# Kernel tuning notes

Hardware: AMD Instinct MI355X
Metric: run time of the kernel (lower is better)

## Reference

```python
import jax, jax.numpy as jnp
import numpy as np

B, N, HID, HEADS, NCT, GDIM = 8, 1024, 1024, 16, 32, 128
HD = HID // HEADS  # head_dim = 64
SCALE = float(np.sqrt(HD))


def setup_inputs() -> dict:
    key = jax.random.key(0)
    ks = jax.random.split(key, 20)
    def lin(k, fan_in, shape):
        bound = 1.0 / np.sqrt(fan_in)
        return jax.random.uniform(k, shape, jnp.float32, -bound, bound)
    return {
        "x": jax.random.normal(ks[0], (B, N, HID), jnp.float32),
        "cancer_type": jax.random.randint(ks[1], (B,), 0, NCT),
        "graph_context": jax.random.normal(ks[2], (B, GDIM), jnp.float32),
        "attn_mask": jnp.zeros((B, N), dtype=bool),
        # projections (stored as [in, out] so y = x @ W + b)
        "Wq": lin(ks[3], HID, (HID, HID)), "bq": lin(ks[4], HID, (HID,)),
        "Wk": lin(ks[5], HID, (HID, HID)), "bk": lin(ks[6], HID, (HID,)),
        "Wv": lin(ks[7], HID, (HID, HID)), "bv": lin(ks[8], HID, (HID,)),
        "Wo": lin(ks[9], HID, (HID, HID)), "bo": lin(ks[10], HID, (HID,)),
        # embeddings
        "ct_bias_emb": jax.random.normal(ks[11], (NCT, HEADS), jnp.float32),
        "ct_key_emb": jax.random.normal(ks[12], (NCT, HID), jnp.float32),
        # graph_attn_bias MLP: graph_dim -> 2*heads -> heads (ELU between)
        "Wg1": lin(ks[13], GDIM, (GDIM, 2 * HEADS)), "bg1": lin(ks[14], GDIM, (2 * HEADS,)),
        "Wg2": lin(ks[15], 2 * HEADS, (2 * HEADS, HEADS)), "bg2": lin(ks[16], 2 * HEADS, (HEADS,)),
        # graph_key_mod: Linear(graph_dim, hidden) + ELU
        "Wgk": lin(ks[17], GDIM, (GDIM, HID)), "bgk": lin(ks[18], GDIM, (HID,)),
    }


def reference(x, cancer_type, graph_context, attn_mask,
              Wq, bq, Wk, bk, Wv, bv, Wo, bo,
              ct_bias_emb, ct_key_emb, Wg1, bg1, Wg2, bg2, Wgk, bgk):
    Bc, Nc, _ = x.shape
    # projections -> (B, H, N, D)
    def split_heads(t):
        return t.reshape(Bc, Nc, HEADS, HD).transpose(0, 2, 1, 3)
    q = split_heads(x @ Wq + bq)
    k = split_heads(x @ Wk + bk)
    v = split_heads(x @ Wv + bv)
    # additive key modulations, broadcast over N: (B, H, 1, D)
    ct_key = ct_key_emb[cancer_type].reshape(Bc, 1, HEADS, HD).transpose(0, 2, 1, 3)
    g_key = jax.nn.elu(graph_context @ Wgk + bgk).reshape(Bc, 1, HEADS, HD).transpose(0, 2, 1, 3)
    k = k + ct_key + g_key
    # scores (B, H, N, N)
    attn = jnp.einsum("bhqd,bhkd->bhqk", q, k) / SCALE
    ct_bias = ct_bias_emb[cancer_type]  # (B, H)
    g_bias = (jax.nn.elu(graph_context @ Wg1 + bg1) @ Wg2 + bg2)  # (B, H)
    attn = attn + (ct_bias + g_bias)[:, :, None, None]
    attn = jnp.where(attn_mask[:, None, None, :], -jnp.inf, attn)
    attn = jax.nn.softmax(attn, axis=-1)
    out = jnp.einsum("bhqk,bhkd->bhqd", attn, v)
    out = out.transpose(0, 2, 1, 3).reshape(Bc, Nc, HID)
    return out @ Wo + bo
```

## Files before the change

kernel.cpp:

```cpp
#include <hip/hip_runtime.h>

typedef unsigned short u16;
typedef __attribute__((ext_vector_type(4))) unsigned short u16x4;
typedef __attribute__((ext_vector_type(2))) unsigned u32x2;
typedef __attribute__((ext_vector_type(8))) __bf16 bf16x8;
typedef __attribute__((ext_vector_type(2))) __bf16 bf16x2;
typedef __attribute__((ext_vector_type(4))) float f32x4;

#define DEV __device__ __forceinline__

DEV u16 f2b(float f) {
    union { float f; unsigned u; } v; v.f = f;
    unsigned r = v.u + 0x7FFFu + ((v.u >> 16) & 1u);
    return (u16)(r >> 16);
}
DEV unsigned pk2(float a, float b) {
    bf16x2 t; t.x = (__bf16)a; t.y = (__bf16)b;
    union { bf16x2 v; unsigned u; } c; c.v = t; return c.u;
}
DEV u16 cvt1(float f) {
    __bf16 h = (__bf16)f;
    union { __bf16 h; u16 u; } c; c.h = h; return c.u;
}

DEV void gl_lds16(const u16* g, const u16* l) {
    __builtin_amdgcn_global_lo\
ad_lds(
        (__attribute__((address_space(1))) void*)(unsigned long long)g,
        (__attribute__((address_space(3))) void*)(unsigned long long)l,
        16, 0, 0);
}

__global__ __launch_bounds__(256) void k_prep(const float* __restrict__ xf, u16* __restrict__ xb,
                                              const float* w0, const float* w1,
                                              const float* w2, const float* w3,
                                              u16* __restrict__ dst)
{
    __shared__ u16 t[64][68];
    int bx = blockIdx.x;
    if (bx < 8192) {
        size_t base = (size_t)bx * 1024 + threadIdx.x * 4;
        float4 v = *(const float4*)&xf[base];
        u16x4 o; o.x = f2b(v.x); o.y = f2b(v.y); o.z = f2b(v.z); o.w = f2b(v.w);
        *(u16x4*)&xb[base] = o;
        return;
    }
    bx -= 8192;
    int z = bx >> 8, tile = bx & 255;
    const float* src = z == 0 ? w0 : z == 1 ? w1 : z == 2 ? w2 : w3;
    u16* d = dst + (size_t)z * 1048576;
    int tx = threadIdx.x & 15, ty = threadIdx.x >> 4;
    int c0 = (tile & 15) * 64, r0 = (tile >> 4) * 64;
#pragma unroll
    for (int i = 0; i < 4; i++) {
        int r = ty + i * 16;
        float4 v = *(const float4*)&src[(size_t)(r0 + r) * 1024 + c0 + tx * 4];
        t[r][tx * 4 + 0] = f2b(v.x); t[r][tx * 4 + 1] = f2b(v.y);
        t[r][tx * 4 + 2] = f2b(v.z); t[r][tx * 4 + 3] = f2b(v.w);
    }
    __syncthreads();
#pragma unroll
    for (int i = 0; i < 4; i++) {
        int cl = ty + i * 16;
        u16x4 v;
        v.x = t[tx * 4 + 0][cl];
        v.y = t[tx * 4 + 1][cl];
        v.z = t[tx * 4 + 2][cl];
        v.w = t[tx * 4 + 3][cl];
        *(u16x4*)&d[(size_t)(c0 + cl) * 1024 + r0 + tx * 4] = v;
    }
}

DEV void gemm128(const u16* __restrict__ A, const u16* __restrict__ BT,
                 const float* __restrict__ bias,
                 u16* __restrict__ Cb, float* __restrict__ Cf,
                 int N, int K, int m0, int n0, int mode, float oscale,
                 u16* As, u16* Bs)
{
    const int tid = threadIdx.x;
    const int w = tid >> 6, lane = tid & 63, quad = lane >> 4, l16 = lane & 15;
    const int wr = w >> 1, wc = w & 1;
    f32x4 acc[4][4] = {};
    const int NS = K >> 5;

    int soff[2], ldst[2];
#pragma unroll
    for (int i = 0; i < 2; i++) {
        int L = (w * 2 + i) * 512 + lane * 8;
        int pr = L >> 6, cp = (L >> 3) & 7;
        int c = cp ^ (pr & 7);
        int r = pr * 2 + (c >> 2);
        soff[i] = r * K + (c & 3) * 8;
        ldst[i] = (w * 2 + i) * 512;
    }
    const u16* Ap = A + (size_t)m0 * K;
    const u16* Bp = BT + (size_t)n0 * K;

    int aoff[4], boff[4];
#pragma unroll
    for (int mi = 0; mi < 4; mi++) {
        int row = wr * 64 + mi * 16 + l16;
        aoff[mi] = (row >> 1) * 64 + (((((row & 1) << 2) | quad) ^ ((row >> 1) & 7)) << 3);
        int rowb = wc * 64 + mi * 16 + l16;
        boff[mi] = (rowb >> 1) * 64 + (((((rowb & 1) << 2) | quad) ^ ((rowb >> 1) & 7)) << 3);
    }

#pragma unroll
    for (int i = 0; i < 2; i++) {
        gl_lds16(Ap + soff[i], As + ldst[i]);
        gl_lds16(Bp + soff[i], Bs + ldst[i]);
    }
    __syncthreads();

    for (int s = 0; s < NS; s++) {
        const u16* curA = As + (s & 1) * 4096;
        const u16* curB = Bs + (s & 1) * 4096;
        if (s + 1 < NS) {
            int kk = (s + 1) * 32;
            u16* nA = As + ((s + 1) & 1) * 4096;
            u16* nB = Bs + ((s + 1) & 1) * 4096;
#pragma unroll
            for (int i = 0; i < 2; i++) {
                gl_lds16(Ap + soff[i] + kk, nA + ldst[i]);
                gl_lds16(Bp + soff[i] + kk, nB + ldst[i]);
            }
        }
        bf16x8 a[4], b[4];
#pragma unroll
        for (int mi = 0; mi < 4; mi++) a[mi] = *(const bf16x8*)&curA[aoff[mi]];
#pragma unroll
        for (int ni = 0; ni < 4; ni++) b[ni] = *(const bf16x8*)&curB[boff[ni]];
#pragma unroll
        for (int mi = 0; mi < 4; mi++)
#pragma unroll
            for (int ni = 0; ni < 4; ni++)
                acc[mi][ni] = __builtin_amdgcn_mfma_f32_16x16x32_bf16(a[mi], b[ni], acc[mi][ni], 0, 0, 0);
        __syncthreads();
    }

    float bs[4];
#pragma unroll
    for (int ni = 0; ni < 4; ni++)
        bs[ni] = bias[n0 + wc * 64 + ni * 16 + l16];

    if (mode == 0) {
#pragma unroll
        for (int mi = 0; mi < 4; mi++) {
            int row = m0 + wr * 64 + mi * 16 + quad * 4;
#pragma unroll
            for (int ni = 0; ni < 4; ni++) {
                int col = n0 + wc * 64 + ni * 16 + l16;
#pragma unroll
                for (int r2 = 0; r2 < 4; r2++)
                    Cb[(size_t)(row + r2) * N + col] = f2b((acc[mi][ni][r2] + bs[ni]) * oscale);
            }
        }
    } else if (mode == 1) {
        int bb = m0 >> 10;
        int nbase = (m0 & 1023) + wr * 64;
#pragma unroll
        for (int mi = 0; mi < 4; mi++) {
            int nrow = nbase + mi * 16 + quad * 4;
#pragma unroll
            for (int ni = 0; ni < 4; ni++) {
                int col = n0 + wc * 64 + ni * 16 + l16;
                int hh = col >> 6, dd = col & 63;
                u16x4 pk;
                pk.x = f2b(acc[mi][ni][0] + bs[ni]);
                pk.y = f2b(acc[mi][ni][1] + bs[ni]);
                pk.z = f2b(acc[mi][ni][2] + bs[ni]);
                pk.w = f2b(acc[mi][ni][3] + bs[ni]);
                *(u16x4*)&Cb[(size_t)(bb * 16 + hh) * 65536 + (size_t)dd * 1024 + nrow] = pk;
            }
        }
    } else {
#pragma unroll
        for (int mi = 0; mi < 4; mi++) {
            int row = m0 + wr * 64 + mi * 16 + quad * 4;
#pragma unroll
            for (int ni = 0; ni < 4; ni++) {
                int col = n0 + wc * 64 + ni * 16 + l16;
#pragma unroll
                for (int r2 = 0; r2 < 4; r2++)
                    Cf[(size_t)(row + r2) * N + col] = acc[mi][ni][r2] + bs[ni];
            }
        }
    }
}

__global__ __launch_bounds__(256, 4) void k_qkv(const u16* __restrict__ x, const u16* __restrict__ WT,
                                                const float* __restrict__ bq, const float* __restrict__ bk,
                                                const float* __restrict__ bv,
                                                u16* __restrict__ QK, u16* __restrict__ Vt)
{
    __shared__ u16 As[8192], Bs[8192];
    int sel = blockIdx.x >> 3;
    const float* bias = sel == 0 ? bq : (sel == 1 ? bk : bv);
    u16* C = sel == 2 ? Vt : QK + (size_t)sel * 8388608;
    float sc = sel == 0 ? 0.18033688011f : 1.0f;
    gemm128(x, WT + (size_t)sel * 1048576, bias, C, (float*)0,
            1024, 1024, blockIdx.y * 128, (blockIdx.x & 7) * 128, sel == 2 ? 1 : 0, sc, As, Bs);
}

__global__ __launch_bounds__(256, 4) void k_out(const u16* __restrict__ A, const u16* __restrict__ WoT,
                                                const float* __restrict__ bo, float* __restrict__ C)
{
    __shared__ u16 As[8192], Bs[8192];
    gemm128(A, WoT, bo, (u16*)0, C, 1024, 1024, blockIdx.y * 128, blockIdx.x * 128, 2, 1.0f, As, Bs);
}

__global__ __launch_bounds__(256, 3) void k_attn(const u16* __restrict__ Q, const u16* __restrict__ K,
                                                 const u16* __restrict__ Vt, u16* __restrict__ O)
{
    __shared__ u16 lds[25600];
    const int tid = threadIdx.x, w = tid >> 6, lane = tid & 63, quad = lane >> 4, l16 = lane & 15;
    const int bh = blockIdx.y, b = bh >> 4, h = bh & 15;
    const int q0 = blockIdx.x * 128;
    const u16* Qp = Q + ((size_t)b * 1024 + q0) * 1024 + h * 64;
    const u16* Kp = K + (size_t)b * 1048576 + h * 64;
    const u16* Vp = Vt + (size_t)bh * 65536;
    u16* Op = O + ((size_t)b * 1024 + q0) * 1024 + h * 64;
    u16* Pw = lds + 16384 + w * 2304;

#pragma unroll
    for (int i = 0; i < 4; i++) {
        int p = (w * 4 + i) * 64 + lane;
        int row = p >> 3, c = (p & 7) ^ (row & 7);
        gl_lds16(Qp + (size_t)row * 1024 + c * 8, lds + (w * 4 + i) * 512);
    }
    __syncthreads();
    bf16x8 qa[2][2];
#pragma unroll
    for (int ni = 0; ni < 2; ni++)
#pragma unroll
        for (int d2 = 0; d2 < 2; d2++)
            qa[ni][d2] = *(const bf16x8*)&lds[(w * 32 + ni * 16 + l16) * 64 + ((d2 * 4 + quad) ^ (l16 & 7)) * 8];
#pragma unroll
    for (int i = 0; i < 2; i++) {
        int p = (w * 2 + i) * 64 + lane;
        int row = p >> 3, c = (p & 7) ^ (row & 7);
        gl_lds16(Kp + (size_t)row * 1024 + c * 8, lds + 8192 + (w * 2 + i) * 512);
        gl_lds16(Vp + (size_t)row * 1024 + c * 8, lds + 8192 + 4096 + (w * 2 + i) * 512);
    }
    __syncthreads();

    f32x4 acc_o[2][4] = {};
    float l_acc[2] = {0.f, 0.f};

    for (int kt = 0; kt < 16; kt++) {
        const u16* buf = lds + (((kt & 1) ^ 1) << 13);
        if (kt < 15) {
            int k0n = (kt + 1) * 64;
            u16* dst = lds + ((kt & 1) << 13);
#pragma unroll
            for (int i = 0; i < 2; i++) {
                int p = (w * 2 + i) * 64 + lane;
                int row = p >> 3, c = (p & 7) ^ (row & 7);
                gl_lds16(Kp + (size_t)(k0n + row) * 1024 + c * 8, dst + (w * 2 + i) * 512);
                gl_lds16(Vp + (size_t)row * 1024 + k0n + c * 8, dst + 4096 + (w * 2 + i) * 512);
            }
        }

        f32x4 s[4][2] = {};
#pragma unroll
        for (int d2 = 0; d2 < 2; d2++) {
            bf16x8 ka[4];
#pragma unroll
            for (int mi = 0; mi < 4; mi++)
                ka[mi] = *(const bf16x8*)&buf[(mi * 16 + l16) * 64 + ((d2 * 4 + quad) ^ (l16 & 7)) * 8];
#pragma unroll
            for (int mi = 0; mi < 4; mi++)
#pragma unroll
                for (int ni = 0; ni < 2; ni++)
                    s[mi][ni] = __builtin_amdgcn_mfma_f32_16x16x32_bf16(ka[mi], qa[ni][d2], s[mi][ni], 0, 0, 0);
        }

#pragma unroll
        for (int ni = 0; ni < 2; ni++) {
            float part = 0.f;
#pragma unroll
            for (int mi = 0; mi < 4; mi++) {
                float e0 = __builtin_amdgcn_exp2f(s[mi][ni][0]);
                float e1 = __builtin_amdgcn_exp2f(s[mi][ni][1]);
                float e2 = __builtin_amdgcn_exp2f(s[mi][ni][2]);
                float e3 = __builtin_amdgcn_exp2f(s[mi][ni][3]);
                part += (e0 + e1) + (e2 + e3);
                u32x2 pk; pk.x = pk2(e0, e1); pk.y = pk2(e2, e3);
                *(u32x2*)&Pw[(ni * 16 + l16) * 72 + mi * 16 + quad * 4] = pk;
            }
            part += __shfl_xor(part, 16);
            part += __shfl_xor(part, 32);
            l_acc[ni] += part;
        }

#pragma unroll
        for (int ks = 0; ks < 2; ks++) {
            bf16x8 pa[2], vb[4];
#pragma unroll
            for (int ni = 0; ni < 2; ni++)
                pa[ni] = *(const bf16x8*)&Pw[(ni * 16 + l16) * 72 + ks * 32 + quad * 8];
#pragma unroll
            for (int di = 0; di < 4; di++)
                vb[di] = *(const bf16x8*)&buf[4096 + (di * 16 + l16) * 64 + ((ks * 4 + quad) ^ (l16 & 7)) * 8];
#pragma unroll
            for (int ni = 0; ni < 2; ni++)
#pragma unroll
                for (int di = 0; di < 4; di++)
                    acc_o[ni][di] = __builtin_amdgcn_mfma_f32_16x16x32_bf16(pa[ni], vb[di], acc_o[ni][di], 0, 0, 0);
        }
        __syncthreads();
    }

#pragma unroll
    for (int ni = 0; ni < 2; ni++) {
#pragma unroll
        for (int r = 0; r < 4; r++) {
            float inv = __builtin_amdgcn_rcpf(__shfl(l_acc[ni], quad * 4 + r));
            int row = w * 32 + ni * 16 + quad * 4 + r;
#pragma unroll
            for (int di = 0; di < 4; di++)
                Op[(size_t)row * 1024 + di * 16 + l16] = cvt1(acc_o[ni][di][r] * inv);
        }
    }
}

extern "C" void kernel_launch(void* const* d_in, const int* in_sizes, int n_in,
                              void* d_out, int out_size, void* d_ws, size_t ws_size,
                              hipStream_t stream)
{
    (void)in_sizes; (void)n_in; (void)out_size; (void)ws_size;
    const float* xf  = (const float*)d_in[0];
    const float* Wqf = (const float*)d_in[4];  const float* bqf = (const float*)d_in[5];
    const float* Wkf = (const float*)d_in[6];  const float* bkf = (const float*)d_in[7];
    const float* Wvf = (const float*)d_in[8];  const float* bvf = (const float*)d_in[9];
    const float* Wof = (const float*)d_in[10]; const float* bof = (const float*)d_in[11];

    u16* ws  = (u16*)d_ws;
    u16* Qw  = ws;
    u16* Kw  = ws + (size_t)8388608;
    u16* Vtw = ws + (size_t)16777216;
    u16* WT  = ws + (size_t)25165824;
    u16* xb  = ws + (size_t)29360128;
    u16* AO  = xb;

    k_prep<<<9216, 256, 0, stream>>>(xf, xb, Wqf, Wkf, Wvf, Wof, WT);
    k_qkv<<<dim3(24, 64), 256, 0, stream>>>(xb, WT, bqf, bkf, bvf, Qw, Vtw);
    k_attn<<<dim3(8, 128), 256, 0, stream>>>(Qw, Kw, Vtw, AO);
    k_out<<<dim3(8, 64), 256, 0, stream>>>(AO, WT + (size_t)3145728, bof, (float*)d_out);
}
```

Baseline: 270.3 us.

## Transpose MFMA operands for vectorized epilogue stores and compute softmax row sums via MFMA

The GEMM epilogue for the Q/K and output projections swaps the MFMA operand order, so each lane holds four consecutive output columns. This allows packed 8-byte bf16 and 16-byte float4 stores plus vector bias loads in place of scalar strided stores. In attention, the P·V MFMA is also transposed for vectorized output writes, and the softmax denominator is accumulated by an extra MFMA against a ones vector, replacing the shuffle reductions. The mode becomes a template parameter and the GEMM occupancy hint rises from 4 to 5; the extra MFMA adds matrix work and the occupancy change may force register spills.

```diff
diff --git a/kernel.cpp b/kernel.cpp
--- a/kernel.cpp
+++ b/kernel.cpp
@@ -18,14 +18,9 @@
     bf16x2 t; t.x = (__bf16)a; t.y = (__bf16)b;
     union { bf16x2 v; unsigned u; } c; c.v = t; return c.u;
 }
-DEV u16 cvt1(float f) {
-    __bf16 h = (__bf16)f;
-    union { __bf16 h; u16 u; } c; c.h = h; return c.u;
-}
 
 DEV void gl_lds16(const u16* g, const u16* l) {
-    __builtin_amdgcn_global_lo\
-ad_lds(
+    __builtin_amdgcn_global_load_lds(
         (__attribute__((address_space(1))) void*)(unsigned long long)g,
         (__attribute__((address_space(3))) void*)(unsigned long long)l,
         16, 0, 0);
@@ -71,10 +66,11 @@
     }
 }
 
+template <int MODE>
 DEV void gemm128(const u16* __restrict__ A, const u16* __restrict__ BT,
                  const float* __restrict__ bias,
                  u16* __restrict__ Cb, float* __restrict__ Cf,
-                 int N, int K, int m0, int n0, int mode, float oscale,
+                 int N, int K, int m0, int n0, float oscale,
                  u16* As, u16* Bs)
 {
     const int tid = threadIdx.x;
@@ -130,32 +126,27 @@
         for (int mi = 0; mi < 4; mi++) a[mi] = *(const bf16x8*)&curA[aoff[mi]];
 #pragma unroll
         for (int ni = 0; ni < 4; ni++) b[ni] = *(const bf16x8*)&curB[boff[ni]];
-#pragma unroll
-        for (int mi = 0; mi < 4; mi++)
+        if (MODE == 1) {
+#pragma unroll
+            for (int mi = 0; mi < 4; mi++)
+#pragma unroll
+                for (int ni = 0; ni < 4; ni++)
+                    acc[mi][ni] = __builtin_amdgcn_mfma_f32_16x16x32_bf16(a[mi], b[ni], acc[mi][ni], 0, 0, 0);
+        } else {
 #pragma unroll
             for (int ni = 0; ni < 4; ni++)
-                acc[mi][ni] = __builtin_amdgcn_mfma_f32_16x16x32_bf16(a[mi], b[ni], acc[mi][ni], 0, 0, 0);
+#pragma unroll
+                for (int mi = 0; mi < 4; mi++)
+                    acc[ni][mi] = __builtin_amdgcn_mfma_f32_16x16x32_bf16(b[ni], a[mi], acc[ni][mi], 0, 0, 0);
+        }
         __syncthreads();
     }
 
-    float bs[4];
-#pragma unroll
-    for (int ni = 0; ni < 4; ni++)
-        bs[ni] = bias[n0 + wc * 64 + ni * 16 + l16];
-
-    if (mode == 0) {
-#pragma unroll
-        for (int mi = 0; mi < 4; mi++) {
-            int row = m0 + wr * 64 + mi * 16 + quad * 4;
-#pragma unroll
-            for (int ni = 0; ni < 4; ni++) {
-                int col = n0 + wc * 64 + ni * 16 + l16;
-#pragma unroll
-                for (int r2 = 0; r2 < 4; r2++)
-                    Cb[(size_t)(row + r2) * N + col] = f2b((acc[mi][ni][r2] + bs[ni]) * oscale);
-            }
-        }
-    } else if (mode == 1) {
+    if (MODE == 1) {
+        float bs[4];
+#pragma unroll
+        for (int ni = 0; ni < 4; ni++)
+            bs[ni] = bias[n0 + wc * 64 + ni * 16 + l16];
         int bb = m0 >> 10;
         int nbase = (m0 & 1023) + wr * 64;
 #pragma unroll
@@ -175,38 +166,53 @@
         }
     } else {
 #pragma unroll
-        for (int mi = 0; mi < 4; mi++) {
-            int row = m0 + wr * 64 + mi * 16 + quad * 4;
-#pragma unroll
-            for (int ni = 0; ni < 4; ni++) {
-                int col = n0 + wc * 64 + ni * 16 + l16;
-#pragma unroll
-                for (int r2 = 0; r2 < 4; r2++)
-                    Cf[(size_t)(row + r2) * N + col] = acc[mi][ni][r2] + bs[ni];
-            }
-        }
-    }
-}
-
-__global__ __launch_bounds__(256, 4) void k_qkv(const u16* __restrict__ x, const u16* __restrict__ WT,
+        for (int ni = 0; ni < 4; ni++) {
+            int cb = n0 + wc * 64 + ni * 16 + quad * 4;
+            float4 bv = *(const float4*)&bias[cb];
+#pragma unroll
+            for (int mi = 0; mi < 4; mi++) {
+                int t = m0 + wr * 64 + mi * 16 + l16;
+                if (MODE == 0) {
+                    u16x4 pk;
+                    pk.x = f2b((acc[ni][mi][0] + bv.x) * oscale);
+                    pk.y = f2b((acc[ni][mi][1] + bv.y) * oscale);
+                    pk.z = f2b((acc[ni][mi][2] + bv.z) * oscale);
+                    pk.w = f2b((acc[ni][mi][3] + bv.w) * oscale);
+                    *(u16x4*)&Cb[(size_t)t * N + cb] = pk;
+                } else {
+                    float4 o;
+                    o.x = acc[ni][mi][0] + bv.x; o.y = acc[ni][mi][1] + bv.y;
+                    o.z = acc[ni][mi][2] + bv.z; o.w = acc[ni][mi][3] + bv.w;
+                    *(float4*)&Cf[(size_t)t * N + cb] = o;
+                }
+            }
+        }
+    }
+}
+
+__global__ __launch_bounds__(256, 5) void k_qkv(const u16* __restrict__ x, const u16* __restrict__ WT,
                                                 const float* __restrict__ bq, const float* __restrict__ bk,
                                                 const float* __restrict__ bv,
                                                 u16* __restrict__ QK, u16* __restrict__ Vt)
 {
     __shared__ u16 As[8192], Bs[8192];
     int sel = blockIdx.x >> 3;
-    const float* bias = sel == 0 ? bq : (sel == 1 ? bk : bv);
-    u16* C = sel == 2 ? Vt : QK + (size_t)sel * 8388608;
-    float sc = sel == 0 ? 0.18033688011f : 1.0f;
-    gemm128(x, WT + (size_t)sel * 1048576, bias, C, (float*)0,
-            1024, 1024, blockIdx.y * 128, (blockIdx.x & 7) * 128, sel == 2 ? 1 : 0, sc, As, Bs);
-}
-
-__global__ __launch_bounds__(256, 4) void k_out(const u16* __restrict__ A, const u16* __restrict__ WoT,
+    int m0 = blockIdx.y * 128, n0 = (blockIdx.x & 7) * 128;
+    if (sel == 2) {
+        gemm128<1>(x, WT + (size_t)2 * 1048576, bv, Vt, (float*)0, 1024, 1024, m0, n0, 1.0f, As, Bs);
+    } else {
+        const float* bias = sel == 0 ? bq : bk;
+        float sc = sel == 0 ? 0.18033688011f : 1.0f;
+        gemm128<0>(x, WT + (size_t)sel * 1048576, bias, QK + (size_t)sel * 8388608, (float*)0,
+                   1024, 1024, m0, n0, sc, As, Bs);
+    }
+}
+
+__global__ __launch_bounds__(256, 5) void k_out(const u16* __restrict__ A, const u16* __restrict__ WoT,
                                                 const float* __restrict__ bo, float* __restrict__ C)
 {
     __shared__ u16 As[8192], Bs[8192];
-    gemm128(A, WoT, bo, (u16*)0, C, 1024, 1024, blockIdx.y * 128, blockIdx.x * 128, 2, 1.0f, As, Bs);
+    gemm128<2>(A, WoT, bo, (u16*)0, C, 1024, 1024, blockIdx.y * 128, blockIdx.x * 128, 1.0f, As, Bs);
 }
 
 __global__ __launch_bounds__(256, 3) void k_attn(const u16* __restrict__ Q, const u16* __restrict__ K,
@@ -244,8 +250,12 @@
     }
     __syncthreads();
 
-    f32x4 acc_o[2][4] = {};
-    float l_acc[2] = {0.f, 0.f};
+    bf16x8 ones;
+#pragma unroll
+    for (int j = 0; j < 8; j++) ones[j] = (__bf16)1.0f;
+
+    f32x4 acc_o[4][2] = {};
+    f32x4 acc_l[2] = {};
 
     for (int kt = 0; kt < 16; kt++) {
         const u16* buf = lds + (((kt & 1) ^ 1) << 13);
@@ -276,22 +286,16 @@
         }
 
 #pragma unroll
-        for (int ni = 0; ni < 2; ni++) {
-            float part = 0.f;
+        for (int ni = 0; ni < 2; ni++)
 #pragma unroll
             for (int mi = 0; mi < 4; mi++) {
                 float e0 = __builtin_amdgcn_exp2f(s[mi][ni][0]);
                 float e1 = __builtin_amdgcn_exp2f(s[mi][ni][1]);
                 float e2 = __builtin_amdgcn_exp2f(s[mi][ni][2]);
                 float e3 = __builtin_amdgcn_exp2f(s[mi][ni][3]);
-                part += (e0 + e1) + (e2 + e3);
                 u32x2 pk; pk.x = pk2(e0, e1); pk.y = pk2(e2, e3);
                 *(u32x2*)&Pw[(ni * 16 + l16) * 72 + mi * 16 + quad * 4] = pk;
             }
-            part += __shfl_xor(part, 16);
-            part += __shfl_xor(part, 32);
-            l_acc[ni] += part;
-        }
 
 #pragma unroll
         for (int ks = 0; ks < 2; ks++) {
@@ -303,23 +307,26 @@
             for (int di = 0; di < 4; di++)
                 vb[di] = *(const bf16x8*)&buf[4096 + (di * 16 + l16) * 64 + ((ks * 4 + quad) ^ (l16 & 7)) * 8];
 #pragma unroll
-            for (int ni = 0; ni < 2; ni++)
+            for (int ni = 0; ni < 2; ni++) {
+                acc_l[ni] = __builtin_amdgcn_mfma_f32_16x16x32_bf16(ones, pa[ni], acc_l[ni], 0, 0, 0);
 #pragma unroll
                 for (int di = 0; di < 4; di++)
-                    acc_o[ni][di] = __builtin_amdgcn_mfma_f32_16x16x32_bf16(pa[ni], vb[di], acc_o[ni][di], 0, 0, 0);
+                    acc_o[di][ni] = __builtin_amdgcn_mfma_f32_16x16x32_bf16(vb[di], pa[ni], acc_o[di][ni], 0, 0, 0);
+            }
         }
         __syncthreads();
     }
 
 #pragma unroll
     for (int ni = 0; ni < 2; ni++) {
-#pragma unroll
-        for (int r = 0; r < 4; r++) {
-            float inv = __builtin_amdgcn_rcpf(__shfl(l_acc[ni], quad * 4 + r));
-            int row = w * 32 + ni * 16 + quad * 4 + r;
-#pragma unroll
-            for (int di = 0; di < 4; di++)
-                Op[(size_t)row * 1024 + di * 16 + l16] = cvt1(acc_o[ni][di][r] * inv);
+        float inv = __builtin_amdgcn_rcpf(acc_l[ni][0]);
+        int q = w * 32 + ni * 16 + l16;
+#pragma unroll
+        for (int di = 0; di < 4; di++) {
+            u32x2 po;
+            po.x = pk2(acc_o[di][ni][0] * inv, acc_o[di][ni][1] * inv);
+            po.y = pk2(acc_o[di][ni][2] * inv, acc_o[di][ni][3] * inv);
+            *(u32x2*)&Op[(size_t)q * 1024 + di * 16 + quad * 4] = po;
         }
     }
 }
```

Result: slower. 298.7 us (+10.5%).
